# Kernel optimization log

Hardware: AMD Instinct MI355X
Metric: run time of the kernel (lower is better)

## Reference

```python
import jax, jax.numpy as jnp
import numpy as np

N_NODES = 50000
N_EDGES = 800000
EMB = 96
LAYER_NUM = 3


def setup_inputs() -> dict:
    key = jax.random.key(0)
    k1, k2, k3, k4 = jax.random.split(key, 4)
    X = jax.random.normal(k1, (N_NODES, EMB), dtype=jnp.float32)
    vals = jax.random.uniform(k2, (N_EDGES,), dtype=jnp.float32)
    rows = jax.random.randint(k3, (N_EDGES,), 0, N_NODES, dtype=jnp.int64)
    cols = jax.random.randint(k4, (N_EDGES,), 0, N_NODES, dtype=jnp.int64)
    return {"X": X, "vals": vals, "rows": rows, "cols": cols}


def reference(X, vals, rows, cols):
    # Eval-mode GNN forward: dropout layers are identity, graph is not dropped.
    # Per layer: agg = A @ ego  (COO SpMM via gather + segment_sum), then
    # ego = agg + agg * ego (elementwise gating). Output = mean over all layers.
    N = X.shape[0]
    ego = X
    acc = X  # running sum of layer embeddings (layer 0 = X)
    for _ in range(LAYER_NUM):
        # SpMM: gather source features, scale by edge values, scatter-add to rows
        msgs = vals[:, None] * ego[cols]          # [E, D]
        agg = jax.ops.segment_sum(msgs, rows, num_segments=N)  # [N, D]
        ego = agg + agg * ego
        acc = acc + ego
    return acc / jnp.asarray(LAYER_NUM + 1, dtype=X.dtype)
```

## Files before the change

kernel.cpp:

```cpp
#include <hip/hip_runtime.h>
#include <hip/hip_bf16.h>


#define N_NODES 50000
#define N_EDGES 800000
#define EMB 96
#define C16 12
#define TPR 6
#define LAYER_NUM 3
#define PAD 64
#define NCHUNK (N_NODES * C16)

#define NBUCK 196
#define RPB 256
#define CAP 5000
#define CNT_PAD 16
#define EDGE_BLOCKS 782
#define CONV_BLOCKS 2344

__device__ __forceinline__ float bflo(unsigned u) { return __uint_as_float(u << 16); }
__device__ __forceinline__ float bfhi(unsigned u) { return __uint_as_float(u & 0xffff0000u); }

__device__ __forceinline__ void fma_bf8(float* s, float v, const uint4& u) {
    s[0] = fmaf(v, bflo(u.x), s[0]);
    s[1] = fmaf(v, bfhi(u.x), s[1]);
    s[2] = fmaf(v, bflo(u.y), s[2]);
    s[3] = fmaf(v, bfhi(u.y), s[3]);
    s[4] = fmaf(v, bflo(u.z), s[4]);
    s[5] = fmaf(v, bfhi(u.z), s[5]);
    s[6] = fmaf(v, bflo(u.w), s[6]);
    s[7] = fmaf(v, bfhi(u.w), s[7]);
}

__device__ __forceinline__ void unpack8(float* d, const uint4& u) {
    d[0] = bflo(u.x); d[1] = bfhi(u.x);
    d[2] = bflo(u.y); d[3] = bfhi(u.y);
    d[4] = bflo(u.z); d[5] = bfhi(u.z);
    d[6] = bflo(u.w); d[7] = bfhi(u.w);
}

__device__ __forceinline__ unsigned packbf(float a, float b) {
    unsigned ua = __float_as_uint(a);
    unsigned ub = __float_as_uint(b);
    ua = (ua + 0x7fffu + ((ua >> 16) & 1u)) >> 16;
    ub = (ub + 0x7fffu + ((ub >> 16) & 1u)) & 0xffff0000u;
    return ua | ub;
}

__global__ void setup_kernel(const float4* __restrict__ X4,
                             uint4* __restrict__ Xb,
                             const int4* __restrict__ rows4,
                             const int4* __restrict__ cols4,
                             const float4* __restrict__ vals4,
                             int* __restrict__ bucket_cnt,
                             uint2* __restrict__ bucket_buf) {
    __shared__ int hist[NBUCK];
    __shared__ int gbase[NBUCK];
    int tid = threadIdx.x;

    if (blockIdx.x < EDGE_BLOCKS) {
        for (int i = tid; i < NBUCK; i += 256) hist[i] = 0;
        __syncthreads();

        int e = blockIdx.x * 256 + tid;
        bool act = (e < N_EDGES / 4);
        int4 r, c; float4 v;
        int b0 = 0, b1 = 0, b2 = 0, b3 = 0;
        int k0 = 0, k1 = 0, k2 = 0, k3 = 0;
        if (act) {
            r = rows4[e]; c = cols4[e]; v = vals4[e];
            b0 = r.x >> 8; b1 = r.y >> 8; b2 = r.z >> 8; b3 = r.w >> 8;
            k0 = atomicAdd(&hist[b0], 1);
            k1 = atomicAdd(&hist[b1], 1);
            k2 = atomicAdd(&hist[b2], 1);
            k3 = atomicAdd(&hist[b3], 1);
        }
        __syncthreads();

        for (int i = tid; i < NBUCK; i += 256)
            gbase[i] = atomicAdd(&bucket_cnt[i * CNT_PAD], hist[i]);
        __syncthreads();

        if (act) {
            uint2 p;
            int d;
            d = gbase[b0] + k0;
            if (d < CAP) {
                p.x = (unsigned)c.x | ((unsigned)(r.x & 255) << 24);
                p.y = __float_as_uint(v.x);
                bucket_buf[b0 * CAP + d] = p;
            }
            d = gbase[b1] + k1;
            if (d < CAP) {
                p.x = (unsigned)c.y | ((unsigned)(r.y & 255) << 24);
                p.y = __float_as_uint(v.y);
                bucket_buf[b1 * CAP + d] = p;
            }
            d = gbase[b2] + k2;
            if (d < CAP) {
                p.x = (unsigned)c.z | ((unsigned)(r.z & 255) << 24);
                p.y = __float_as_uint(v.z);
                bucket_buf[b2 * CAP + d] = p;
            }
            d = gbase[b3] + k3;
            if (d < CAP) {
                p.x = (unsigned)c.w | ((unsigned)(r.w & 255) << 24);
                p.y = __float_as_uint(v.w);
                bucket_buf[b3 * CAP + d] = p;
            }
        }
    } else {
        int chunk = (blockIdx.x - EDGE_BLOCKS) * 256 + tid;
        if (chunk < NCHUNK) {
            float4 a = X4[chunk * 2];
            float4 b = X4[chunk * 2 + 1];
            uint4 o;
            o.x = packbf(a.x, a.y);
            o.y = packbf(a.z, a.w);
            o.z = packbf(b.x, b.y);
            o.w = packbf(b.z, b.w);
            Xb[chunk] = o;
        }
    }
}

__global__ void ell_build_kernel(const int* __restrict__ bucket_cnt,
                                 const uint2* __restrict__ bucket_buf,
                                 int2* __restrict__ ell,
                                 int* __restrict__ cnt) {
    __shared__ int lc[RPB];
    int b = blockIdx.x;
    int tid = threadIdx.x;
    if (tid < RPB) lc[tid] = 0;
    __syncthreads();

    int n = bucket_cnt[b * CNT_PAD];
    if (n > CAP) n = CAP;
    const uint2* buf = bucket_buf + b * CAP;
    for (int i = tid; i < n; i += 512) {
        uint2 rec = buf[i];
        int rl = rec.x >> 24;
        int slot = atomicAdd(&lc[rl], 1);
        if (slot < PAD) {
            int2 p;
            p.x = (int)(rec.x & 0x00ffffffu);
            p.y = (int)rec.y;
            ell[(b * RPB + rl) * PAD + slot] = p;
        }
    }
    __syncthreads();
    if (tid < RPB) {
        int row = b * RPB + tid;
        if (row < N_NODES) {
            int d = lc[tid];
            cnt[row] = (d > PAD) ? PAD : d;
        }
    }
}

template <int MODE>
__global__ void spmm_fused_kernel(const uint4* __restrict__ ego_in,
                                  uint4* __restrict__ ego_out,
                                  const int* __restrict__ cnt,
                                  const int4* __restrict__ ell4,
                                  const uint4* __restrict__ xb,
                                  const uint4* __restrict__ e1v,
                                  float4* __restrict__ acc) {
    int tid = blockIdx.x * blockDim.x + threadIdx.x;
    if (tid >= N_NODES * TPR) return;
    int row = tid / TPR;
    int ct  = tid % TPR;

    int deg = cnt[row];
    const int4* ep = ell4 + row * (PAD / 2);

    float s0[8] = {0.f, 0.f, 0.f, 0.f, 0.f, 0.f, 0.f, 0.f};
    float s1[8] = {0.f, 0.f, 0.f, 0.f, 0.f, 0.f, 0.f, 0.f};

    int j = 0;
    for (; j + 4 <= deg; j += 4) {
        int4 pA = ep[j >> 1];
        int4 pB = ep[(j >> 1) + 1];
        const uint4* b0 = ego_in + pA.x * C16;
        const uint4* b1 = ego_in + pA.z * C16;
        const uint4* b2 = ego_in + pB.x * C16;
        const uint4* b3 = ego_in + pB.z * C16;
        uint4 x0a = b0[ct], x0b = b0[ct + TPR];
        uint4 x1a = b1[ct], x1b = b1[ct + TPR];
        uint4 x2a = b2[ct], x2b = b2[ct + TPR];
        uint4 x3a = b3[ct], x3b = b3[ct + TPR];
        float v0 = __int_as_float(pA.y);
        float v1 = __int_as_float(pA.w);
        float v2 = __int_as_float(pB.y);
        float v3 = __int_as_float(pB.w);
        fma_bf8(s0, v0, x0a); fma_bf8(s1, v0, x0b);
        fma_bf8(s0, v1, x1a); fma_bf8(s1, v1, x1b);
        fma_bf8(s0, v2, x2a); fma_bf8(s1, v2, x2b);
        fma_bf8(s0, v3, x3a); fma_bf8(s1, v3, x3b);
    }
    for (; j + 2 <= deg; j += 2) {
        int4 pA = ep[j >> 1];
        const uint4* b0 = ego_in + pA.x * C16;
        const uint4* b1 = ego_in + pA.z * C16;
        uint4 x0a = b0[ct], x0b = b0[ct + TPR];
        uint4 x1a = b1[ct], x1b = b1[ct + TPR];
        float v0 = __int_as_float(pA.y);
        float v1 = __int_as_float(pA.w);
        fma_bf8(s0, v0, x0a); fma_bf8(s1, v0, x0b);
        fma_bf8(s0, v1, x1a); fma_bf8(s1, v1, x1b);
    }
    if (j < deg) {
        int2 p = ((const int2*)ell4)[row * PAD + j];
        const uint4* b0 = ego_in + p.x * C16;
        uint4 x0a = b0[ct], x0b = b0[ct + TPR];
        float v0 = __int_as_float(p.y);
        fma_bf8(s0, v0, x0a); fma_bf8(s1, v0, x0b);
    }

    int ib = row * C16 + ct;
    uint4 ea = ego_in[ib];
    uint4 eb = ego_in[ib + TPR];
    float e0[8], e1[8];
    unpack8(e0, ea);
    unpack8(e1, eb);
    float n0[8], n1[8];
#pragma unroll
    for (int k = 0; k < 8; ++k) {
        n0[k] = fmaf(s0[k], e0[k], s0[k]);
        n1[k] = fmaf(s1[k], e1[k], s1[k]);
    }

    if (MODE == 0) {
        uint4 oa, ob;
        oa.x = packbf(n0[0], n0[1]); oa.y = packbf(n0[2], n0[3]);
        oa.z = packbf(n0[4], n0[5]); oa.w = packbf(n0[6], n0[7]);
        ob.x = packbf(n1[0], n1[1]); ob.y = packbf(n1[2], n1[3]);
        ob.z = packbf(n1[4], n1[5]); ob.w = packbf(n1[6], n1[7]);
        ego_out[ib]       = oa;
        ego_out[ib + TPR] = ob;
    } else {
        float x0[8], x1[8], f0[8], f1[8];
        unpack8(x0, xb[ib]);
        unpack8(x1, xb[ib + TPR]);
        unpack8(f0, e1v[ib]);
        unpack8(f1, e1v[ib + TPR]);
        int ia = row * (EMB / 4) + ct * 2;
        float4 a0, a1, a2, a3;
        a0.x = (x0[0] + f0[0] + e0[0] + n0[0]) * 0.25f;
        a0.y = (x0[1] + f0[1] + e0[1] + n0[1]) * 0.25f;
        a0.z = (x0[2] + f0[2] + e0[2] + n0[2]) * 0.25f;
        a0.w = (x0[3] + f0[3] + e0[3] + n0[3]) * 0.25f;
        a1.x = (x0[4] + f0[4] + e0[4] + n0[4]) * 0.25f;
        a1.y = (x0[5] + f0[5] + e0[5] + n0[5]) * 0.25f;
        a1.z = (x0[6] + f0[6] + e0[6] + n0[6]) * 0.25f;
        a1.w = (x0[7] + f0[7] + e0[7] + n0[7]) * 0.25f;
        a2.x = (x1[0] + f1[0] + e1[0] + n1[0]) * 0.25f;
        a2.y = (x1[1] + f1[1] + e1[1] + n1[1]) * 0.25f;
        a2.z = (x1[2] + f1[2] + e1[2] + n1[2]) * 0.25f;
        a2.w = (x1[3] + f1[3] + e1[3] + n1[3]) * 0.25f;
        a3.x = (x1[4] + f1[4] + e1[4] + n1[4]) * 0.25f;
        a3.y = (x1[5] + f1[5] + e1[5] + n1[5]) * 0.25f;
        a3.z = (x1[6] + f1[6] + e1[6] + n1[6]) * 0.25f;
        a3.w = (x1[7] + f1[7] + e1[7] + n1[7]) * 0.25f;
        acc[ia]      = a0;
        acc[ia + 1]  = a1;
        acc[ia + 12] = a2;
        acc[ia + 13] = a3;
    }
}

extern "C" void kernel_launch(void* const* d_in, const int* in_sizes, int n_in,
                              void* d_out, int out_size, void* d_ws, size_t ws_size,
                              hipStream_t stream) {
    const float* X    = (const float*)d_in[0];
    const float* vals = (const float*)d_in[1];
    const int*   rows = (const int*)d_in[2];
    const int*   cols = (const int*)d_in[3];

    const size_t nodeb_bytes = (size_t)NCHUNK * sizeof(uint4);
    const size_t ell_bytes   = (size_t)N_NODES * PAD * sizeof(int2);
    const size_t cnt_bytes   = (size_t)N_NODES * sizeof(int);

    float* acc = (float*)d_out;

    char* w = (char*)d_ws;
    uint4* Xb    = (uint4*)w;  w += nodeb_bytes;
    uint4* ego_a = (uint4*)w;  w += nodeb_bytes;
    uint4* ego_b = (uint4*)w;  w += nodeb_bytes;
    int2*  ell   = (int2*)w;   w += ell_bytes;
    int*   cnt   = (int*)w;    w += cnt_bytes;

    uint2* bucket_buf = (uint2*)ego_a;
    int*   bucket_cnt = (int*)ego_b;

    hipMemsetAsync(bucket_cnt, 0, NBUCK * CNT_PAD * sizeof(int), stream);

    setup_kernel<<<EDGE_BLOCKS + CONV_BLOCKS, 256, 0, stream>>>(
        (const float4*)X, Xb,
        (const int4*)rows, (const int4*)cols, (const float4*)vals,
        bucket_cnt, bucket_buf);

    ell_build_kernel<<<NBUCK, 512, 0, stream>>>(bucket_cnt, bucket_buf, ell, cnt);

    const int blocks = (N_NODES * TPR + 255) / 256;

    spmm_fused_kernel<0><<<blocks, 256, 0, stream>>>(
        Xb, ego_a, cnt, (const int4*)ell, nullptr, nullptr, nullptr);
    spmm_fused_kernel<0><<<blocks, 256, 0, stream>>>(
        ego_a, ego_b, cnt, (const int4*)ell, nullptr, nullptr, nullptr);
    spmm_fused_kernel<1><<<blocks, 256, 0, stream>>>(
        ego_b, nullptr, cnt, (const int4*)ell, Xb, ego_a, (float4*)acc);
}
```

Baseline: 189.9 us.

## Fuse all stages into one persistent cooperative kernel with grid syncs

Replaces the memset plus five separate kernel launches with a single cooperative persistent kernel. Blocks loop over the virtual blocks of each stage, and stages are separated by grid.sync. This is meant to remove launch gaps and inter-kernel drain overhead. In exchange it adds grid-wide barrier costs and limits the grid to the occupancy-derived size, which may reduce latency hiding in the gather-heavy SpMM phases. The ELL build also changes from 512 to 256 threads per block.

Result: slower. 481.2 us (+153.3%).

```diff
diff --git a/kernel.cpp b/kernel.cpp
--- a/kernel.cpp
+++ b/kernel.cpp
@@ -1,5 +1,8 @@
 #include <hip/hip_runtime.h>
 #include <hip/hip_bf16.h>
+#include <hip/hip_cooperative_groups.h>
+
+namespace cg = cooperative_groups;
 
 
 #define N_NODES 50000
@@ -17,6 +20,8 @@
 #define CNT_PAD 16
 #define EDGE_BLOCKS 782
 #define CONV_BLOCKS 2344
+#define VB_SETUP (EDGE_BLOCKS + CONV_BLOCKS)
+#define VB_SPMM ((N_NODES * TPR + 255) / 256)
 
 __device__ __forceinline__ float bflo(unsigned u) { return __uint_as_float(u << 16); }
 __device__ __forceinline__ float bfhi(unsigned u) { return __uint_as_float(u & 0xffff0000u); }
@@ -47,22 +52,21 @@
     return ua | ub;
 }
 
-__global__ void setup_kernel(const float4* __restrict__ X4,
-                             uint4* __restrict__ Xb,
-                             const int4* __restrict__ rows4,
-                             const int4* __restrict__ cols4,
-                             const float4* __restrict__ vals4,
-                             int* __restrict__ bucket_cnt,
-                             uint2* __restrict__ bucket_buf) {
-    __shared__ int hist[NBUCK];
-    __shared__ int gbase[NBUCK];
-    int tid = threadIdx.x;
-
-    if (blockIdx.x < EDGE_BLOCKS) {
+
+__device__ void setup_vb(int vb, int tid,
+                         const float4* __restrict__ X4,
+                         uint4* __restrict__ Xb,
+                         const int4* __restrict__ rows4,
+                         const int4* __restrict__ cols4,
+                         const float4* __restrict__ vals4,
+                         int* __restrict__ bucket_cnt,
+                         uint2* __restrict__ bucket_buf,
+                         int* hist, int* gbase) {
+    if (vb < EDGE_BLOCKS) {
         for (int i = tid; i < NBUCK; i += 256) hist[i] = 0;
         __syncthreads();
 
-        int e = blockIdx.x * 256 + tid;
+        int e = vb * 256 + tid;
         bool act = (e < N_EDGES / 4);
         int4 r, c; float4 v;
         int b0 = 0, b1 = 0, b2 = 0, b3 = 0;
@@ -109,8 +113,9 @@
                 bucket_buf[b3 * CAP + d] = p;
             }
         }
+        __syncthreads();
     } else {
-        int chunk = (blockIdx.x - EDGE_BLOCKS) * 256 + tid;
+        int chunk = (vb - EDGE_BLOCKS) * 256 + tid;
         if (chunk < NCHUNK) {
             float4 a = X4[chunk * 2];
             float4 b = X4[chunk * 2 + 1];
@@ -124,20 +129,19 @@
     }
 }
 
-__global__ void ell_build_kernel(const int* __restrict__ bucket_cnt,
-                                 const uint2* __restrict__ bucket_buf,
-                                 int2* __restrict__ ell,
-                                 int* __restrict__ cnt) {
-    __shared__ int lc[RPB];
-    int b = blockIdx.x;
-    int tid = threadIdx.x;
-    if (tid < RPB) lc[tid] = 0;
+__device__ void ellbuild_vb(int b, int tid,
+                            const int* __restrict__ bucket_cnt,
+                            const uint2* __restrict__ bucket_buf,
+                            int2* __restrict__ ell,
+                            int* __restrict__ cnt,
+                            int* lc) {
+    lc[tid] = 0;
     __syncthreads();
 
     int n = bucket_cnt[b * CNT_PAD];
     if (n > CAP) n = CAP;
     const uint2* buf = bucket_buf + b * CAP;
-    for (int i = tid; i < n; i += 512) {
+    for (int i = tid; i < n; i += 256) {
         uint2 rec = buf[i];
         int rl = rec.x >> 24;
         int slot = atomicAdd(&lc[rl], 1);
@@ -149,27 +153,25 @@
         }
     }
     __syncthreads();
-    if (tid < RPB) {
-        int row = b * RPB + tid;
-        if (row < N_NODES) {
-            int d = lc[tid];
-            cnt[row] = (d > PAD) ? PAD : d;
-        }
-    }
+    int row = b * RPB + tid;
+    if (row < N_NODES) {
+        int d = lc[tid];
+        cnt[row] = (d > PAD) ? PAD : d;
+    }
+    __syncthreads();
 }
 
 template <int MODE>
-__global__ void spmm_fused_kernel(const uint4* __restrict__ ego_in,
-                                  uint4* __restrict__ ego_out,
-                                  const int* __restrict__ cnt,
-                                  const int4* __restrict__ ell4,
-                                  const uint4* __restrict__ xb,
-                                  const uint4* __restrict__ e1v,
-                                  float4* __restrict__ acc) {
-    int tid = blockIdx.x * blockDim.x + threadIdx.x;
-    if (tid >= N_NODES * TPR) return;
-    int row = tid / TPR;
-    int ct  = tid % TPR;
+__device__ void spmm_task(int t,
+                          const uint4* __restrict__ ego_in,
+                          uint4* __restrict__ ego_out,
+                          const int* __restrict__ cnt,
+                          const int4* __restrict__ ell4,
+                          const uint4* __restrict__ xb,
+                          const uint4* __restrict__ e1v,
+                          float4* __restrict__ acc) {
+    int row = t / TPR;
+    int ct  = t % TPR;
 
     int deg = cnt[row];
     const int4* ep = ell4 + row * (PAD / 2);
@@ -269,19 +271,98 @@
     }
 }
 
+
+__global__ void fused_kernel(const float4* __restrict__ X4,
+                             uint4* __restrict__ Xb,
+                             const int4* __restrict__ rows4,
+                             const int4* __restrict__ cols4,
+                             const float4* __restrict__ vals4,
+                             int* __restrict__ bucket_cnt,
+                             uint2* __restrict__ bucket_buf,
+                             int2* __restrict__ ell,
+                             int* __restrict__ cnt,
+                             uint4* __restrict__ ego_a,
+                             uint4* __restrict__ ego_b,
+                             float4* __restrict__ acc) {
+    cg::grid_group grid = cg::this_grid();
+    __shared__ int hist[NBUCK];
+    __shared__ int gbase[NBUCK];
+    __shared__ int lc[RPB];
+
+    const int tid = threadIdx.x;
+    const int nb  = gridDim.x;
+
+    for (int i = blockIdx.x * 256 + tid; i < NBUCK * CNT_PAD; i += nb * 256)
+        bucket_cnt[i] = 0;
+    grid.sync();
+
+    for (int vb = blockIdx.x; vb < VB_SETUP; vb += nb)
+        setup_vb(vb, tid, X4, Xb, rows4, cols4, vals4, bucket_cnt, bucket_buf,
+                 hist, gbase);
+    grid.sync();
+
+    for (int b = blockIdx.x; b < NBUCK; b += nb)
+        ellbuild_vb(b, tid, bucket_cnt, bucket_buf, ell, cnt, lc);
+    grid.sync();
+
+    for (int t = blockIdx.x * 256 + tid; t < N_NODES * TPR; t += nb * 256)
+        spmm_task<0>(t, Xb, ego_a, cnt, (const int4*)ell, nullptr, nullptr, nullptr);
+    grid.sync();
+    for (int t = blockIdx.x * 256 + tid; t < N_NODES * TPR; t += nb * 256)
+        spmm_task<0>(t, ego_a, ego_b, cnt, (const int4*)ell, nullptr, nullptr, nullptr);
+    grid.sync();
+    for (int t = blockIdx.x * 256 + tid; t < N_NODES * TPR; t += nb * 256)
+        spmm_task<1>(t, ego_b, nullptr, cnt, (const int4*)ell, Xb, ego_a, acc);
+}
+
+
+__global__ void setup_kernel(const float4* __restrict__ X4,
+                             uint4* __restrict__ Xb,
+                             const int4* __restrict__ rows4,
+                             const int4* __restrict__ cols4,
+                             const float4* __restrict__ vals4,
+                             int* __restrict__ bucket_cnt,
+                             uint2* __restrict__ bucket_buf) {
+    __shared__ int hist[NBUCK];
+    __shared__ int gbase[NBUCK];
+    setup_vb(blockIdx.x, threadIdx.x, X4, Xb, rows4, cols4, vals4,
+             bucket_cnt, bucket_buf, hist, gbase);
+}
+
+__global__ void ell_build_kernel(const int* __restrict__ bucket_cnt,
+                                 const uint2* __restrict__ bucket_buf,
+                                 int2* __restrict__ ell,
+                                 int* __restrict__ cnt) {
+    __shared__ int lc[RPB];
+    ellbuild_vb(blockIdx.x, threadIdx.x, bucket_cnt, bucket_buf, ell, cnt, lc);
+}
+
+template <int MODE>
+__global__ void spmm_fused_kernel(const uint4* __restrict__ ego_in,
+                                  uint4* __restrict__ ego_out,
+                                  const int* __restrict__ cnt,
+                                  const int4* __restrict__ ell4,
+                                  const uint4* __restrict__ xb,
+                                  const uint4* __restrict__ e1v,
+                                  float4* __restrict__ acc) {
+    int t = blockIdx.x * blockDim.x + threadIdx.x;
+    if (t < N_NODES * TPR)
+        spmm_task<MODE>(t, ego_in, ego_out, cnt, ell4, xb, e1v, acc);
+}
+
 extern "C" void kernel_launch(void* const* d_in, const int* in_sizes, int n_in,
                               void* d_out, int out_size, void* d_ws, size_t ws_size,
                               hipStream_t stream) {
-    const float* X    = (const float*)d_in[0];
-    const float* vals = (const float*)d_in[1];
-    const int*   rows = (const int*)d_in[2];
-    const int*   cols = (const int*)d_in[3];
+    const float4* X4    = (const float4*)d_in[0];
+    const float4* vals4 = (const float4*)d_in[1];
+    const int4*   rows4 = (const int4*)d_in[2];
+    const int4*   cols4 = (const int4*)d_in[3];
 
     const size_t nodeb_bytes = (size_t)NCHUNK * sizeof(uint4);
     const size_t ell_bytes   = (size_t)N_NODES * PAD * sizeof(int2);
     const size_t cnt_bytes   = (size_t)N_NODES * sizeof(int);
 
-    float* acc = (float*)d_out;
+    float4* acc = (float4*)d_out;
 
     char* w = (char*)d_ws;
     uint4* Xb    = (uint4*)w;  w += nodeb_bytes;
@@ -293,21 +374,43 @@
     uint2* bucket_buf = (uint2*)ego_a;
     int*   bucket_cnt = (int*)ego_b;
 
-    hipMemsetAsync(bucket_cnt, 0, NBUCK * CNT_PAD * sizeof(int), stream);
-
-    setup_kernel<<<EDGE_BLOCKS + CONV_BLOCKS, 256, 0, stream>>>(
-        (const float4*)X, Xb,
-        (const int4*)rows, (const int4*)cols, (const float4*)vals,
-        bucket_cnt, bucket_buf);
-
-    ell_build_kernel<<<NBUCK, 512, 0, stream>>>(bucket_cnt, bucket_buf, ell, cnt);
-
-    const int blocks = (N_NODES * TPR + 255) / 256;
-
-    spmm_fused_kernel<0><<<blocks, 256, 0, stream>>>(
-        Xb, ego_a, cnt, (const int4*)ell, nullptr, nullptr, nullptr);
-    spmm_fused_kernel<0><<<blocks, 256, 0, stream>>>(
-        ego_a, ego_b, cnt, (const int4*)ell, nullptr, nullptr, nullptr);
-    spmm_fused_kernel<1><<<blocks, 256, 0, stream>>>(
-        ego_b, nullptr, cnt, (const int4*)ell, Xb, ego_a, (float4*)acc);
-}
+    static int coopGrid = -1;
+    if (coopGrid < 0) {
+        int occ = 0;
+        if (hipOccupancyMaxActiveBlocksPerMultiprocessor(&occ, fused_kernel,
+                                                         256, 0) != hipSuccess)
+            occ = 0;
+        if (occ < 1) {
+            coopGrid = 0;
+        } else {
+            long g = (long)occ * 256;
+            if (g > VB_SPMM) g = VB_SPMM;
+            coopGrid = (int)g;
+        }
+    }
+
+    hipError_t err = hipErrorUnknown;
+    if (coopGrid > 0) {
+        void* args[] = {
+            (void*)&X4, (void*)&Xb, (void*)&rows4, (void*)&cols4, (void*)&vals4,
+            (void*)&bucket_cnt, (void*)&bucket_buf, (void*)&ell, (void*)&cnt,
+            (void*)&ego_a, (void*)&ego_b, (void*)&acc
+        };
+        err = hipLaunchCooperativeKernel((const void*)fused_kernel,
+                                         dim3(coopGrid), dim3(256),
+                                         args, 0, stream);
+    }
+
+    if (err != hipSuccess) {
+        hipMemsetAsync(bucket_cnt, 0, NBUCK * CNT_PAD * sizeof(int), stream);
+        setup_kernel<<<VB_SETUP, 256, 0, stream>>>(
+            X4, Xb, rows4, cols4, vals4, bucket_cnt, bucket_buf);
+        ell_build_kernel<<<NBUCK, 256, 0, stream>>>(bucket_cnt, bucket_buf, ell, cnt);
+        spmm_fused_kernel<0><<<VB_SPMM, 256, 0, stream>>>(
+            Xb, ego_a, cnt, (const int4*)ell, nullptr, nullptr, nullptr);
+        spmm_fused_kernel<0><<<VB_SPMM, 256, 0, stream>>>(
+            ego_a, ego_b, cnt, (const int4*)ell, nullptr, nullptr, nullptr);
+        spmm_fused_kernel<1><<<VB_SPMM, 256, 0, stream>>>(
+            ego_b, nullptr, cnt, (const int4*)ell, Xb, ego_a, acc);
+    }
+}
```

## Gather int8-quantized node features with per-chunk bf16 scales in SpMM

Applied to the files above, without the earlier changes.

Adds an int8 copy of each node's embedding: 16 values per thread-chunk plus a bf16 scale, packed into 128 bytes per row. The setup kernel and each intermediate layer write this copy, and the SpMM gathers read it instead of the 192-byte bf16 rows. The goal is to cut the bytes moved by the random neighbor gathers, which dominate the cost. In exchange it adds quantization work, an extra small scale load per edge, and extra writes, and it loses accuracy by using 8-bit features in aggregation, which may break the tolerance.

New measurement: 174.5 us (median of 2 runs). 1.09x faster.

```diff
diff --git a/kernel.cpp b/kernel.cpp
--- a/kernel.cpp
+++ b/kernel.cpp
@@ -7,30 +7,21 @@
 #define EMB 96
 #define C16 12
 #define TPR 6
-#define LAYER_NUM 3
 #define PAD 64
 #define NCHUNK (N_NODES * C16)
+#define Q8U4 8
 
 #define NBUCK 196
 #define RPB 256
 #define CAP 5000
 #define CNT_PAD 16
 #define EDGE_BLOCKS 782
-#define CONV_BLOCKS 2344
+#define CONV_BLOCKS ((N_NODES * TPR + 255) / 256)
+#define VB_SETUP (EDGE_BLOCKS + CONV_BLOCKS)
+#define VB_SPMM ((N_NODES * TPR + 255) / 256)
 
 __device__ __forceinline__ float bflo(unsigned u) { return __uint_as_float(u << 16); }
 __device__ __forceinline__ float bfhi(unsigned u) { return __uint_as_float(u & 0xffff0000u); }
-
-__device__ __forceinline__ void fma_bf8(float* s, float v, const uint4& u) {
-    s[0] = fmaf(v, bflo(u.x), s[0]);
-    s[1] = fmaf(v, bfhi(u.x), s[1]);
-    s[2] = fmaf(v, bflo(u.y), s[2]);
-    s[3] = fmaf(v, bfhi(u.y), s[3]);
-    s[4] = fmaf(v, bflo(u.z), s[4]);
-    s[5] = fmaf(v, bfhi(u.z), s[5]);
-    s[6] = fmaf(v, bflo(u.w), s[6]);
-    s[7] = fmaf(v, bfhi(u.w), s[7]);
-}
 
 __device__ __forceinline__ void unpack8(float* d, const uint4& u) {
     d[0] = bflo(u.x); d[1] = bfhi(u.x);
@@ -47,8 +38,54 @@
     return ua | ub;
 }
 
+__device__ __forceinline__ unsigned q8w(const int* m) {
+    return (unsigned)(m[0] & 255) | ((unsigned)(m[1] & 255) << 8) |
+           ((unsigned)(m[2] & 255) << 16) | ((unsigned)(m[3] & 255) << 24);
+}
+
+__device__ __forceinline__ void q8enc(const float* f, uint4* mout,
+                                      unsigned short* sout) {
+    float mx = 0.f;
+#pragma unroll
+    for (int k = 0; k < 16; ++k) mx = fmaxf(mx, fabsf(f[k]));
+    unsigned sb = 0;
+    float inv = 0.f;
+    if (mx > 1e-30f) {
+        float sc = mx * (1.0078125f / 127.0f);
+        unsigned u = __float_as_uint(sc);
+        sb = (u + 0x7fffu + ((u >> 16) & 1u)) >> 16;
+        inv = 1.0f / __uint_as_float(sb << 16);
+    }
+    int m[16];
+#pragma unroll
+    for (int k = 0; k < 16; ++k) {
+        int v = __float2int_rn(f[k] * inv);
+        m[k] = min(127, max(-127, v));
+    }
+    uint4 o;
+    o.x = q8w(m); o.y = q8w(m + 4); o.z = q8w(m + 8); o.w = q8w(m + 12);
+    *mout = o;
+    *sout = (unsigned short)sb;
+}
+
+__device__ __forceinline__ void fma_q8x4(float* s, float c, unsigned w) {
+    s[0] = fmaf(c, (float)((int)(w << 24) >> 24), s[0]);
+    s[1] = fmaf(c, (float)((int)(w << 16) >> 24), s[1]);
+    s[2] = fmaf(c, (float)((int)(w << 8) >> 24), s[2]);
+    s[3] = fmaf(c, (float)((int)w >> 24), s[3]);
+}
+
+__device__ __forceinline__ void fma_q8x16(float* s, float c, const uint4& x) {
+    fma_q8x4(s,      c, x.x);
+    fma_q8x4(s + 4,  c, x.y);
+    fma_q8x4(s + 8,  c, x.z);
+    fma_q8x4(s + 12, c, x.w);
+}
+
+
 __global__ void setup_kernel(const float4* __restrict__ X4,
                              uint4* __restrict__ Xb,
+                             uint4* __restrict__ Xq8,
                              const int4* __restrict__ rows4,
                              const int4* __restrict__ cols4,
                              const float4* __restrict__ vals4,
@@ -110,16 +147,29 @@
             }
         }
     } else {
-        int chunk = (blockIdx.x - EDGE_BLOCKS) * 256 + tid;
-        if (chunk < NCHUNK) {
-            float4 a = X4[chunk * 2];
-            float4 b = X4[chunk * 2 + 1];
-            uint4 o;
-            o.x = packbf(a.x, a.y);
-            o.y = packbf(a.z, a.w);
-            o.z = packbf(b.x, b.y);
-            o.w = packbf(b.z, b.w);
-            Xb[chunk] = o;
+        int th = (blockIdx.x - EDGE_BLOCKS) * 256 + tid;
+        if (th < N_NODES * TPR) {
+            int row = th / TPR;
+            int ct  = th % TPR;
+            const float4* Xr = X4 + row * 24;
+            float4 a = Xr[2 * ct];
+            float4 b = Xr[2 * ct + 1];
+            float4 c = Xr[2 * ct + 12];
+            float4 d = Xr[2 * ct + 13];
+            uint4 oa, ob;
+            oa.x = packbf(a.x, a.y); oa.y = packbf(a.z, a.w);
+            oa.z = packbf(b.x, b.y); oa.w = packbf(b.z, b.w);
+            ob.x = packbf(c.x, c.y); ob.y = packbf(c.z, c.w);
+            ob.z = packbf(d.x, d.y); ob.w = packbf(d.z, d.w);
+            Xb[row * C16 + ct]       = oa;
+            Xb[row * C16 + ct + TPR] = ob;
+            float f[16] = {a.x, a.y, a.z, a.w, b.x, b.y, b.z, b.w,
+                           c.x, c.y, c.z, c.w, d.x, d.y, d.z, d.w};
+            unsigned short sb;
+            uint4 mq;
+            q8enc(f, &mq, &sb);
+            Xq8[row * Q8U4 + ct] = mq;
+            ((unsigned short*)Xq8)[row * 64 + 48 + ct] = sb;
         }
     }
 }
@@ -160,7 +210,9 @@
 
 template <int MODE>
 __global__ void spmm_fused_kernel(const uint4* __restrict__ ego_in,
+                                  const uint4* __restrict__ q8_in,
                                   uint4* __restrict__ ego_out,
+                                  uint4* __restrict__ q8_out,
                                   const int* __restrict__ cnt,
                                   const int4* __restrict__ ell4,
                                   const uint4* __restrict__ xb,
@@ -173,48 +225,42 @@
 
     int deg = cnt[row];
     const int4* ep = ell4 + row * (PAD / 2);
-
-    float s0[8] = {0.f, 0.f, 0.f, 0.f, 0.f, 0.f, 0.f, 0.f};
-    float s1[8] = {0.f, 0.f, 0.f, 0.f, 0.f, 0.f, 0.f, 0.f};
+    const unsigned short* qs = (const unsigned short*)q8_in;
+
+    float s[16] = {0.f, 0.f, 0.f, 0.f, 0.f, 0.f, 0.f, 0.f,
+                   0.f, 0.f, 0.f, 0.f, 0.f, 0.f, 0.f, 0.f};
 
     int j = 0;
     for (; j + 4 <= deg; j += 4) {
         int4 pA = ep[j >> 1];
         int4 pB = ep[(j >> 1) + 1];
-        const uint4* b0 = ego_in + pA.x * C16;
-        const uint4* b1 = ego_in + pA.z * C16;
-        const uint4* b2 = ego_in + pB.x * C16;
-        const uint4* b3 = ego_in + pB.z * C16;
-        uint4 x0a = b0[ct], x0b = b0[ct + TPR];
-        uint4 x1a = b1[ct], x1b = b1[ct + TPR];
-        uint4 x2a = b2[ct], x2b = b2[ct + TPR];
-        uint4 x3a = b3[ct], x3b = b3[ct + TPR];
-        float v0 = __int_as_float(pA.y);
-        float v1 = __int_as_float(pA.w);
-        float v2 = __int_as_float(pB.y);
-        float v3 = __int_as_float(pB.w);
-        fma_bf8(s0, v0, x0a); fma_bf8(s1, v0, x0b);
-        fma_bf8(s0, v1, x1a); fma_bf8(s1, v1, x1b);
-        fma_bf8(s0, v2, x2a); fma_bf8(s1, v2, x2b);
-        fma_bf8(s0, v3, x3a); fma_bf8(s1, v3, x3b);
+        uint4 x0 = q8_in[pA.x * Q8U4 + ct];
+        uint4 x1 = q8_in[pA.z * Q8U4 + ct];
+        uint4 x2 = q8_in[pB.x * Q8U4 + ct];
+        uint4 x3 = q8_in[pB.z * Q8U4 + ct];
+        float c0 = __int_as_float(pA.y) * bflo((unsigned)qs[pA.x * 64 + 48 + ct]);
+        float c1 = __int_as_float(pA.w) * bflo((unsigned)qs[pA.z * 64 + 48 + ct]);
+        float c2 = __int_as_float(pB.y) * bflo((unsigned)qs[pB.x * 64 + 48 + ct]);
+        float c3 = __int_as_float(pB.w) * bflo((unsigned)qs[pB.z * 64 + 48 + ct]);
+        fma_q8x16(s, c0, x0);
+        fma_q8x16(s, c1, x1);
+        fma_q8x16(s, c2, x2);
+        fma_q8x16(s, c3, x3);
     }
     for (; j + 2 <= deg; j += 2) {
         int4 pA = ep[j >> 1];
-        const uint4* b0 = ego_in + pA.x * C16;
-        const uint4* b1 = ego_in + pA.z * C16;
-        uint4 x0a = b0[ct], x0b = b0[ct + TPR];
-        uint4 x1a = b1[ct], x1b = b1[ct + TPR];
-        float v0 = __int_as_float(pA.y);
-        float v1 = __int_as_float(pA.w);
-        fma_bf8(s0, v0, x0a); fma_bf8(s1, v0, x0b);
-        fma_bf8(s0, v1, x1a); fma_bf8(s1, v1, x1b);
+        uint4 x0 = q8_in[pA.x * Q8U4 + ct];
+        uint4 x1 = q8_in[pA.z * Q8U4 + ct];
+        float c0 = __int_as_float(pA.y) * bflo((unsigned)qs[pA.x * 64 + 48 + ct]);
+        float c1 = __int_as_float(pA.w) * bflo((unsigned)qs[pA.z * 64 + 48 + ct]);
+        fma_q8x16(s, c0, x0);
+        fma_q8x16(s, c1, x1);
     }
     if (j < deg) {
         int2 p = ((const int2*)ell4)[row * PAD + j];
-        const uint4* b0 = ego_in + p.x * C16;
-        uint4 x0a = b0[ct], x0b = b0[ct + TPR];
-        float v0 = __int_as_float(p.y);
-        fma_bf8(s0, v0, x0a); fma_bf8(s1, v0, x0b);
+        uint4 x0 = q8_in[p.x * Q8U4 + ct];
+        float c0 = __int_as_float(p.y) * bflo((unsigned)qs[p.x * 64 + 48 + ct]);
+        fma_q8x16(s, c0, x0);
     }
 
     int ib = row * C16 + ct;
@@ -226,8 +272,8 @@
     float n0[8], n1[8];
 #pragma unroll
     for (int k = 0; k < 8; ++k) {
-        n0[k] = fmaf(s0[k], e0[k], s0[k]);
-        n1[k] = fmaf(s1[k], e1[k], s1[k]);
+        n0[k] = fmaf(s[k],     e0[k], s[k]);
+        n1[k] = fmaf(s[8 + k], e1[k], s[8 + k]);
     }
 
     if (MODE == 0) {
@@ -238,6 +284,13 @@
         ob.z = packbf(n1[4], n1[5]); ob.w = packbf(n1[6], n1[7]);
         ego_out[ib]       = oa;
         ego_out[ib + TPR] = ob;
+        float f[16] = {n0[0], n0[1], n0[2], n0[3], n0[4], n0[5], n0[6], n0[7],
+                       n1[0], n1[1], n1[2], n1[3], n1[4], n1[5], n1[6], n1[7]};
+        unsigned short sb;
+        uint4 mq;
+        q8enc(f, &mq, &sb);
+        q8_out[row * Q8U4 + ct] = mq;
+        ((unsigned short*)q8_out)[row * 64 + 48 + ct] = sb;
     } else {
         float x0[8], x1[8], f0[8], f1[8];
         unpack8(x0, xb[ib]);
@@ -278,8 +331,9 @@
     const int*   cols = (const int*)d_in[3];
 
     const size_t nodeb_bytes = (size_t)NCHUNK * sizeof(uint4);
+    const size_t q8_bytes    = (size_t)N_NODES * Q8U4 * sizeof(uint4);
     const size_t ell_bytes   = (size_t)N_NODES * PAD * sizeof(int2);
-    const size_t cnt_bytes   = (size_t)N_NODES * sizeof(int);
+    const size_t cnt_bytes   = 204800;
 
     float* acc = (float*)d_out;
 
@@ -289,25 +343,26 @@
     uint4* ego_b = (uint4*)w;  w += nodeb_bytes;
     int2*  ell   = (int2*)w;   w += ell_bytes;
     int*   cnt   = (int*)w;    w += cnt_bytes;
+    uint4* q8a   = (uint4*)w;  w += q8_bytes;
+    uint4* q8b   = (uint4*)w;  w += q8_bytes;
 
     uint2* bucket_buf = (uint2*)ego_a;
     int*   bucket_cnt = (int*)ego_b;
 
     hipMemsetAsync(bucket_cnt, 0, NBUCK * CNT_PAD * sizeof(int), stream);
 
-    setup_kernel<<<EDGE_BLOCKS + CONV_BLOCKS, 256, 0, stream>>>(
-        (const float4*)X, Xb,
+    setup_kernel<<<VB_SETUP, 256, 0, stream>>>(
+        (const float4*)X, Xb, q8a,
         (const int4*)rows, (const int4*)cols, (const float4*)vals,
         bucket_cnt, bucket_buf);
 
     ell_build_kernel<<<NBUCK, 512, 0, stream>>>(bucket_cnt, bucket_buf, ell, cnt);
 
-    const int blocks = (N_NODES * TPR + 255) / 256;
-
-    spmm_fused_kernel<0><<<blocks, 256, 0, stream>>>(
-        Xb, ego_a, cnt, (const int4*)ell, nullptr, nullptr, nullptr);
-    spmm_fused_kernel<0><<<blocks, 256, 0, stream>>>(
-        ego_a, ego_b, cnt, (const int4*)ell, nullptr, nullptr, nullptr);
-    spmm_fused_kernel<1><<<blocks, 256, 0, stream>>>(
-        ego_b, nullptr, cnt, (const int4*)ell, Xb, ego_a, (float4*)acc);
-}
+    spmm_fused_kernel<0><<<VB_SPMM, 256, 0, stream>>>(
+        Xb, q8a, ego_a, q8b, cnt, (const int4*)ell, nullptr, nullptr, nullptr);
+    spmm_fused_kernel<0><<<VB_SPMM, 256, 0, stream>>>(
+        ego_a, q8b, ego_b, q8a, cnt, (const int4*)ell, nullptr, nullptr, nullptr);
+    spmm_fused_kernel<1><<<VB_SPMM, 256, 0, stream>>>(
+        ego_b, q8a, nullptr, nullptr, cnt, (const int4*)ell, Xb, ego_a,
+        (float4*)acc);
+}
```
